# Kernel optimization log

Hardware: AMD Instinct MI355X
Metric: run time of the kernel (lower is better)

Reference implementation:

```python
import jax, jax.numpy as jnp
import numpy as np
from jax import lax

COUNTER_TARGET = 40
CONV_THRESH = 0.01


def compute_ellipticity(images):
    """images: [B,H,W] -> (e1[B], e2[B]) via iterative adaptive-Gaussian moments."""
    B, H, W = images.shape
    y = jnp.arange(H, dtype=jnp.float32) - H / 2.0 + 0.5
    x = jnp.arange(W, dtype=jnp.float32) - W / 2.0 + 0.5
    Y, X = jnp.meshgrid(y, x, indexing='ij')  # [H,W]
    X = X[None]  # [1,H,W]
    Y = Y[None]
    total = jnp.sum(images, axis=(1, 2))
    image_area = jnp.float32(H * W)

    def cond_fn(c):
        i, ax, ay, axy, mux, muy, psxx, psyy, csxx, csyy, back, e1, e2 = c
        first = jnp.equal(i, 0)
        valid = jnp.logical_not(jnp.any(jnp.isnan(csxx))) & jnp.logical_not(jnp.any(jnp.isnan(csyy)))
        converged = (jnp.max(jnp.abs(csxx - psxx)) < CONV_THRESH) & (jnp.max(jnp.abs(csyy - psyy)) < CONV_THRESH)
        converged = converged & jnp.logical_not(first)
        return (i < COUNTER_TARGET) & valid & (first | jnp.logical_not(converged))

    def body_fn(c):
        i, ax, ay, axy, mux, muy, psxx, psyy, csxx, csyy, back, e1, e2 = c
        ax = jnp.clip(ax, 0.5, 20.0)
        ay = jnp.clip(ay, 0.5, 20.0)
        axy = jnp.clip(axy, -10.0, 10.0)
        Xc = X - mux[:, None, None]
        Yc = Y - muy[:, None, None]
        alpha_denom = jnp.maximum(ax * ay, 1e-8)
        alpha_ratio = jnp.clip(axy / alpha_denom, -0.95, 0.95)
        arb_const = jnp.maximum(2.0 * (1.0 - alpha_ratio ** 2), 1e-8)
        sqrt_term = jnp.maximum(1.0 - alpha_ratio ** 2, 1e-8)
        A = 1.0 / (2.0 * jnp.pi * alpha_denom * jnp.sqrt(sqrt_term))
        A = jnp.clip(A, 1e-10, 1e10)
        ax_sq = jnp.maximum(ax ** 2, 1e-8)
        ay_sq = jnp.maximum(ay ** 2, 1e-8)
        e1t = Xc ** 2 / (arb_const * ax_sq)[:, None, None]
        e2t = Yc ** 2 / (arb_const * ay_sq)[:, None, None]
        e3t = 2.0 * axy[:, None, None] * Xc * Yc / (arb_const * ax_sq * ay_sq)[:, None, None]
        exp_term = jnp.clip(e1t + e2t - e3t, 0.0, 30.0)
        k = A[:, None, None] * jnp.exp(-exp_term)
        k = jnp.where(jnp.isnan(k), 0.0, k)
        k = jnp.where(jnp.isinf(k), 0.0, k)
        img1 = images - back[:, None, None]
        ik = img1 * k
        t1 = jnp.sum(X * Y * ik, axis=(1, 2))
        t2 = jnp.sum(ik, axis=(1, 2))
        t3 = jnp.sum(X * ik, axis=(1, 2))
        t4 = jnp.sum(Y * ik, axis=(1, 2))
        t5 = jnp.sum(X * X * ik, axis=(1, 2))
        t6 = jnp.sum(Y * Y * ik, axis=(1, 2))
        t7 = jnp.sum(k * k, axis=(1, 2))
        t2s = jnp.maximum(jnp.abs(t2), 1e-6)
        t7s = jnp.maximum(t7, 1e-6)
        flux_calc = t2 / t7s
        new_back = jnp.clip((total - flux_calc) / image_area, -1.0, 1.0)
        new_mux = jnp.clip(t3 / t2s, -W / 2.0, W / 2.0)
        new_muy = jnp.clip(t4 / t2s, -H / 2.0, H / 2.0)
        sigxx = t5 / t2s - (t3 / t2s) ** 2
        sigyy = t6 / t2s - (t4 / t2s) ** 2
        sigxy = t1 / t2s - t3 * t4 / (t2s * t2s)
        sigxx = jnp.clip(sigxx, 0.25, 100.0)
        sigyy = jnp.clip(sigyy, 0.25, 100.0)
        sigxy = jnp.clip(sigxy, -50.0, 50.0)
        nax = jnp.sqrt(jnp.clip(sigxx * 2.0, 1.0, 400.0))
        nay = jnp.sqrt(jnp.clip(sigyy * 2.0, 1.0, 400.0))
        naxy = jnp.clip(2.0 * sigxy, -20.0, 20.0)
        denom = jnp.maximum(sigxx + sigyy, 1e-6)
        ne1 = jnp.clip((sigxx - sigyy) / denom, -0.95, 0.95)
        ne2 = jnp.clip(2.0 * sigxy / denom, -0.95, 0.95)
        ne1 = jnp.where(jnp.isnan(ne1), 0.0, ne1)
        ne2 = jnp.where(jnp.isnan(ne2), 0.0, ne2)
        nax = jnp.where(jnp.isnan(nax), 2.0, nax)
        nay = jnp.where(jnp.isnan(nay), 2.0, nay)
        naxy = jnp.where(jnp.isnan(naxy), 0.0, naxy)
        return (i + 1, nax, nay, naxy, new_mux, new_muy, csxx, csyy, sigxx, sigyy, new_back, ne1, ne2)

    def step(c, _):
        cont = cond_fn(c)
        nc = body_fn(c)
        c = jax.tree_util.tree_map(lambda a, b: jnp.where(cont, b, a), c, nc)
        return c, None

    init = (jnp.int32(0),
            jnp.full([B], 2.0), jnp.full([B], 2.0), jnp.zeros([B]),
            jnp.zeros([B]), jnp.zeros([B]),
            jnp.full([B], 4.0), jnp.full([B], 4.0),
            jnp.zeros([B]), jnp.zeros([B]),
            jnp.zeros([B]), jnp.zeros([B]), jnp.zeros([B]))
    final, _ = lax.scan(step, init, None, length=COUNTER_TARGET)
    e1, e2 = final[11], final[12]
    e1 = jnp.where(jnp.isnan(e1) | jnp.isinf(e1), 0.0, e1)
    e2 = jnp.where(jnp.isnan(e2) | jnp.isinf(e2), 0.0, e2)
    return e1, e2


def blur_with_kernel(image, kernel):
    """image [B,H,W,1], kernel [B,kH,kW,1] -> per-sample SAME conv (correlation)."""
    def single(img, ker):
        ker = ker / (jnp.sum(ker) + 1e-6)
        ker = ker[..., None]  # [kH,kW,1,1] HWIO
        out = lax.conv_general_dilated(img[None], ker, window_strides=(1, 1),
                                       padding='SAME',
                                       dimension_numbers=('NHWC', 'HWIO', 'NHWC'))
        return out[0]
    return jax.vmap(single)(image, kernel)


def setup_inputs() -> dict:
    key = jax.random.key(0)
    ks = jax.random.split(key, 5)
    B, H, W, kH = 512, 96, 96, 31
    return {
        'y_pred': jax.random.uniform(ks[0], (B, H, W, 1), dtype=jnp.float32),
        'y_true': jax.random.uniform(ks[1], (B, H, W, 1), dtype=jnp.float32),
        'blurred_img': jax.random.uniform(ks[2], (B, H, W, 2), dtype=jnp.float32),
        'kernel_img': jax.random.uniform(ks[3], (B, kH, kH, 1), dtype=jnp.float32),
        'weight_map': jax.random.uniform(ks[4], (B, H, W, 1), dtype=jnp.float32),
        'current_epoch': 3,
    }


def reference(y_pred, y_true, blurred_img, kernel_img, weight_map, current_epoch):
    weighted_mse = jnp.mean(jnp.square(y_pred - y_true) * weight_map)
    sharp_true = jnp.squeeze(y_true, axis=-1)
    sharp_pred = jnp.squeeze(y_pred, axis=-1)
    e1_t, e2_t = compute_ellipticity(sharp_true)
    e1_p, e2_p = compute_ellipticity(sharp_pred)
    ellip_diff = jnp.mean((e1_t - e1_p) ** 2 + (e2_t - e2_p) ** 2)
    ellip_loss = jnp.clip(ellip_diff, 0.0, 1.0)
    ellip_weight = 0.01 + 0.1 * jnp.float32(min(current_epoch, 4))
    original_blurred = blurred_img[:, :, :, 0:1]
    reblurred = blur_with_kernel(y_pred, kernel_img)
    reblur_loss = jnp.mean(jnp.square(reblurred - original_blurred) * weight_map)
    total_loss = 100.0 * weighted_mse + 100.0 * reblur_loss + ellip_weight * ellip_loss
    return total_loss
```

## Files before the change

### kernel.cpp

```cpp
#include <hip/hip_runtime.h>

#define HW 9216
#define NBATCH 512

__device__ __forceinline__ float clampf(float v, float lo, float hi){ return fminf(fmaxf(v, lo), hi); }

__device__ __forceinline__ float waveSum(float v){
#pragma unroll
  for (int o = 32; o; o >>= 1) v += __shfl_xor(v, o, 64);
  return v;
}

__global__ __launch_bounds__(256) void mse_kernel(const float4* __restrict__ yp,
                                                  const float4* __restrict__ yt,
                                                  const float4* __restrict__ wm,
                                                  float* __restrict__ partial){
  __shared__ float red[4];
  const int tid = threadIdx.x;
  int idx = blockIdx.x * 256 + tid;
  float s = 0.f;
#pragma unroll
  for (int u = 0; u < 9; ++u){
    float4 a = yp[idx], b = yt[idx], w = wm[idx];
    float dx = a.x-b.x, dy = a.y-b.y, dz = a.z-b.z, dw = a.w-b.w;
    s += dx*dx*w.x + dy*dy*w.y + dz*dz*w.z + dw*dw*w.w;
    idx += 131072;
  }
  s = waveSum(s);
  if ((tid & 63) == 0) red[tid >> 6] = s;
  __syncthreads();
  if (tid == 0) partial[blockIdx.x] = red[0]+red[1]+red[2]+red[3];
}

__global__ __launch_bounds__(256)
void fused_kernel(const float* __restrict__ y_true,
                  const float* __restrict__ y_pred,
                  const float* __restrict__ kimg,
                  const float* __restrict__ blurred,
                  const float* __restrict__ wmap,
                  float2* __restrict__ ebuf,
                  float* __restrict__ convp){
  __shared__ float smem[7816];
  typedef __fp16 half2_t __attribute__((ext_vector_type(2)));
  const int tid = threadIdx.x;
  const int bid = blockIdx.x;
  const int g   = bid / 5, r5 = bid - g*5;
  const int wave = tid >> 6, lane = tid & 63;

  if (r5 < 2){
    const int id = g*2 + r5;
    float (*wred)[4] = (float(*)[4])smem;
    float* tred = smem + 28;
    const int d = id >> 9;
    const int b = id & 511;
    const int tx = tid & 31, ty = tid >> 5;

    const float* src = (d ? y_pred : y_true) + (size_t)b * HW + ty * 96 + tx;

    unsigned px2[6][3];
    float tot = 0.f;
#pragma unroll
    for (int jj = 0; jj < 6; ++jj){
#pragma unroll
      for (int c = 0; c < 3; ++c){
        float ve = src[jj*1536 + c*32];
        float vo = src[jj*1536 + 768 + c*32];
        tot += ve + vo;
        half2_t pk = __builtin_amdgcn_cvt_pkrtz(ve, vo);
        unsigned u = __builtin_bit_cast(unsigned, pk);
        asm volatile("" : "+v"(u));
        px2[jj][c] = u;
      }
    }
    tot = waveSum(tot);
    if (lane == 0) tred[wave] = tot;
    __syncthreads();
    float total;
    { float4 t = *reinterpret_cast<const float4*>(&tred[0]); total = (t.x+t.y)+(t.z+t.w); }
    __syncthreads();

    const float Ya00 = (float)ty - 47.5f;
    float Xa[3];
#pragma unroll
    for (int c = 0; c < 3; ++c){ Xa[c] = (float)(tx + 32*c) - 47.5f; }

    float zx=4.f, zy=4.f, axy=0.f, mux=0.f, muy=0.f, back=0.f, e1=0.f, e2=0.f;
    const float LOG2E = 1.4426950408889634f;
    const float NQLO  = -43.280851226668906f;

    for (int it = 0; it < 40; ++it){
      float axyc = clampf(axy, -10.f, 10.f);
      float prod = zx*zy;
      float adn  = sqrtf(prod);
      float rca  = __builtin_amdgcn_rcpf(adn);
      float ar   = clampf(axyc*rca, -0.95f, 0.95f);
      float omr  = fmaf(-ar, ar, 1.f);
      float A    = 0.15915494309189535f * rca * __builtin_amdgcn_rsqf(omr);
      float invq = __builtin_amdgcn_rcpf(2.f*omr*prod);
      float a1 = -LOG2E*zy*invq;
      float a2 = -LOG2E*zx*invq;
      float a3 = (2.f*LOG2E)*axyc*invq;
      float cX2[3], cX3[3];
#pragma unroll
      for (int c = 0; c < 3; ++c){
        float Xc = Xa[c] - mux;
        cX2[c] = a1*Xc*Xc;
        cX3[c] = a3*Xc;
      }
      float S0[3] = {0.f,0.f,0.f}, SY[3] = {0.f,0.f,0.f};
      float tYY = 0.f, tkk = 0.f;
#pragma unroll
      for (int jj = 0; jj < 6; ++jj){
        float Yae = Ya00 + 16.f*jj;
        float Yao = Yae + 8.f;
        float Yce = Yae - muy, Yco = Yao - muy;
        float he = a2*Yce*Yce, ho = a2*Yco*Yco;
        float rse = 0.f, rso = 0.f;
#pragma unroll
        for (int c = 0; c < 3; ++c){
          half2_t pk = __builtin_bit_cast(half2_t, px2[jj][c]);
          float pe = (float)pk.x, po = (float)pk.y;
          {
            float nq = fmaf(cX3[c], Yce, he + cX2[c]);
            float e  = __builtin_amdgcn_exp2f(fminf(fmaxf(nq, NQLO), 0.f));
            float ik = (pe - back)*e;
            S0[c] += ik;  SY[c] = fmaf(Yae, ik, SY[c]);  tkk = fmaf(e, e, tkk);  rse += ik;
          }
          {
            float nq = fmaf(cX3[c], Yco, ho + cX2[c]);
            float e  = __builtin_amdgcn_exp2f(fminf(fmaxf(nq, NQLO), 0.f));
            float ik = (po - back)*e;
            S0[c] += ik;  SY[c] = fmaf(Yao, ik, SY[c]);  tkk = fmaf(e, e, tkk);  rso += ik;
          }
        }
        tYY = fmaf(Yae*Yae, rse, fmaf(Yao*Yao, rso, tYY));
      }
      float tik = S0[0]+S0[1]+S0[2];
      float tX  = fmaf(Xa[2],S0[2], fmaf(Xa[1],S0[1], Xa[0]*S0[0]));
      float tXX = fmaf(Xa[2]*Xa[2],S0[2], fmaf(Xa[1]*Xa[1],S0[1], (Xa[0]*Xa[0])*S0[0]));
      float tY  = SY[0]+SY[1]+SY[2];
      float tXY = fmaf(Xa[2],SY[2], fmaf(Xa[1],SY[1], Xa[0]*SY[0]));
      tXY=waveSum(tXY); tik=waveSum(tik); tX=waveSum(tX); tY=waveSum(tY);
      tXX=waveSum(tXX); tYY=waveSum(tYY); tkk=waveSum(tkk);
      if (lane == 0){
        wred[0][wave]=tXY; wred[1][wave]=tik; wred[2][wave]=tX; wred[3][wave]=tY;
        wred[4][wave]=tXX; wred[5][wave]=tYY; wred[6][wave]=tkk;
      }
      __syncthreads();
      float T[7];
#pragma unroll
      for (int k = 0; k < 7; ++k){
        float4 r = *reinterpret_cast<const float4*>(&wred[k][0]);
        T[k] = (r.x+r.y)+(r.z+r.w);
      }
      __syncthreads();
      float T1=T[0]*A, T2=T[1]*A, T3=T[2]*A, T4=T[3]*A, T5=T[4]*A, T6=T[5]*A, T7=T[6]*A*A;
      float t2s = fmaxf(fabsf(T2), 1e-6f);
      float rt2 = __builtin_amdgcn_rcpf(t2s);
      float flux = T2 * __builtin_amdgcn_rcpf(fmaxf(T7, 1e-6f));
      back = clampf((total - flux) * (1.f/9216.f), -1.f, 1.f);
      float r3 = T3*rt2, r4 = T4*rt2;
      mux = clampf(r3, -48.f, 48.f);
      muy = clampf(r4, -48.f, 48.f);
      float sxx = clampf(T5*rt2 - r3*r3, 0.25f, 100.f);
      float syy = clampf(T6*rt2 - r4*r4, 0.25f, 100.f);
      float sxy = clampf(T1*rt2 - T3*T4*rt2*rt2, -50.f, 50.f);
      zx = clampf(sxx*2.f, 1.f, 400.f);
      zy = clampf(syy*2.f, 1.f, 400.f);
      axy = clampf(2.f*sxy, -20.f, 20.f);
      float rden = __builtin_amdgcn_rcpf(sxx+syy);
      e1 = clampf((sxx-syy)*rden, -0.95f, 0.95f);
      e2 = clampf(2.f*sxy*rden, -0.95f, 0.95f);
    }
    if (tid == 0) ebuf[d*512 + b] = make_float2(e1, e2);
  } else {
    const int cid = g*3 + (r5 - 2);
    float* P   = smem;
    float* red = smem + 7812;
    const int b = cid / 3, h = cid - b*3;
    const int R0 = h * 32;

    const float* img = y_pred + (size_t)b * HW;
    for (int u = tid; u < 62*126; u += 256){
      int pr = u / 126, pc = u - pr*126;
      int ir = R0 - 15 + pr, ic = pc - 15;
      float v = 0.f;
      if ((unsigned)ir < 96u && (unsigned)ic < 96u) v = img[ir*96 + ic];
      P[u] = v;
    }
    const float* kb = kimg + (size_t)b * 961;
    float ks = 0.f;
    for (int u = tid; u < 961; u += 256) ks += kb[u];
    ks = waveSum(ks);
    if (lane == 0) red[wave] = ks;
    __syncthreads();
    const float inv = __fdividef(1.f, (red[0]+red[1]+red[2]+red[3]) + 1e-6f);

    const int strip = tid & 15, rg = tid >> 4;
    const int c0 = strip*6;
    const int r0 = R0 + rg*2;
    float acc[2][6];
#pragma unroll
    for (int q = 0; q < 2; ++q){
#pragma unroll
      for (int j = 0; j < 6; ++j) acc[q][j] = 0.f;
    }

#pragma unroll 1
    for (int s = 0; s < 32; ++s){
      const float2* prow = reinterpret_cast<const float2*>(&P[(rg*2 + s)*126 + c0]);
      {
        float w[22];
#pragma unroll
        for (int m = 0; m < 11; ++m){ float2 v = prow[m]; w[2*m]=v.x; w[2*m+1]=v.y; }
#pragma unroll
        for (int q = 0; q < 2; ++q){
          const int dy = s - q;
          if (dy >= 0 && dy <= 30){
            const float* kr = kb + dy*31;
#pragma unroll
            for (int dx = 0; dx < 16; ++dx){
              const float kv = kr[dx];
              acc[q][0] = fmaf(kv, w[dx+0], acc[q][0]);
              acc[q][1] = fmaf(kv, w[dx+1], acc[q][1]);
              acc[q][2] = fmaf(kv, w[dx+2], acc[q][2]);
              acc[q][3] = fmaf(kv, w[dx+3], acc[q][3]);
              acc[q][4] = fmaf(kv, w[dx+4], acc[q][4]);
              acc[q][5] = fmaf(kv, w[dx+5], acc[q][5]);
            }
          }
        }
      }
      {
        float w2[20];
#pragma unroll
        for (int m = 0; m < 10; ++m){ float2 v = prow[8+m]; w2[2*m]=v.x; w2[2*m+1]=v.y; }
#pragma unroll
        for (int q = 0; q < 2; ++q){
          const int dy = s - q;
          if (dy >= 0 && dy <= 30){
            const float* kr = kb + dy*31;
#pragma unroll
            for (int dx = 16; dx < 31; ++dx){
              const float kv = kr[dx];
              acc[q][0] = fmaf(kv, w2[dx-16+0], acc[q][0]);
              acc[q][1] = fmaf(kv, w2[dx-16+1], acc[q][1]);
              acc[q][2] = fmaf(kv, w2[dx-16+2], acc[q][2]);
              acc[q][3] = fmaf(kv, w2[dx-16+3], acc[q][3]);
              acc[q][4] = fmaf(kv, w2[dx-16+4], acc[q][4]);
              acc[q][5] = fmaf(kv, w2[dx-16+5], acc[q][5]);
            }
          }
        }
      }
    }

    float lsum = 0.f;
#pragma unroll
    for (int q = 0; q < 2; ++q){
#pragma unroll
      for (int j = 0; j < 6; ++j){
        const int rr = r0+q, cc = c0+j;
        const size_t pix = (size_t)b*HW + rr*96 + cc;
        float ov = acc[q][j] * inv;
        float dd = ov - blurred[2*pix];
        lsum = fmaf(dd*dd, wmap[pix], lsum);
      }
    }
    lsum = waveSum(lsum);
    __syncthreads();
    if (lane == 0) red[wave] = lsum;
    __syncthreads();
    if (tid == 0) convp[cid] = red[0]+red[1]+red[2]+red[3];
  }
}

__global__ __launch_bounds__(512) void final_kernel(const float* __restrict__ msep,
                                                    const float* __restrict__ convp,
                                                    const float2* __restrict__ ebuf,
                                                    const int* __restrict__ epoch,
                                                    float* __restrict__ out){
  __shared__ float red[3][8];
  const int tid = threadIdx.x, wave = tid >> 6, lane = tid & 63;
  float a = msep[tid];
  float bsum = convp[tid] + convp[512 + tid] + convp[1024 + tid];
  float2 et = ebuf[tid], ep = ebuf[512 + tid];
  float dx = et.x - ep.x, dy = et.y - ep.y;
  float c = dx*dx + dy*dy;
  a = waveSum(a); bsum = waveSum(bsum); c = waveSum(c);
  if (lane == 0){ red[0][wave]=a; red[1][wave]=bsum; red[2][wave]=c; }
  __syncthreads();
  if (tid == 0){
    float sa=0, sb=0, sc=0;
#pragma unroll
    for (int w = 0; w < 8; ++w){ sa+=red[0][w]; sb+=red[1][w]; sc+=red[2][w]; }
    float mse   = sa / 4718592.f;
    float rebl  = sb / 4718592.f;
    float ediff = clampf(sc / 512.f, 0.f, 1.f);
    int e = *epoch; if (e > 4) e = 4;
    float ew = 0.01f + 0.1f * (float)e;
    out[0] = 100.f*mse + 100.f*rebl + ew*ediff;
  }
}

extern "C" void kernel_launch(void* const* d_in, const int* in_sizes, int n_in,
                              void* d_out, int out_size, void* d_ws, size_t ws_size,
                              hipStream_t stream){
  const float* y_pred  = (const float*)d_in[0];
  const float* y_true  = (const float*)d_in[1];
  const float* blurred = (const float*)d_in[2];
  const float* kimg    = (const float*)d_in[3];
  const float* wmap    = (const float*)d_in[4];
  const int*   epoch   = (const int*)d_in[5];
  float* out = (float*)d_out;
  float* ws  = (float*)d_ws;

  float*  msep  = ws;
  float*  convp = ws + 512;
  float2* ebufp = (float2*)(ws + 2048);

  mse_kernel<<<512, 256, 0, stream>>>((const float4*)y_pred, (const float4*)y_true,
                                      (const float4*)wmap, msep);

  fused_kernel<<<2560, 256, 0, stream>>>(y_true, y_pred, kimg, blurred, wmap,
                                         ebufp, convp);

  final_kernel<<<1, 512, 0, stream>>>(msep, convp, ebufp, epoch, out);
}
```

Before: 360.2 us.

## Split fused kernel into ellipticity and conv kernels, fold MSE into conv

The combined block-interleaved kernel is split into two separate launches, one for the ellipticity iterations and one for the reblur convolution. The weighted MSE term moves into the convolution epilogue, reading y_pred from the shared tile and y_true from global memory, which removes the standalone MSE kernel and its separate pass over the inputs. Splitting means each kernel gets its own register and LDS footprint and so its own occupancy, but the two kernels now run one after the other on the stream instead of overlapping within a single grid.

```diff
diff --git a/kernel.cpp b/kernel.cpp
--- a/kernel.cpp
+++ b/kernel.cpp
@@ -11,295 +11,273 @@
   return v;
 }
 
-__global__ __launch_bounds__(256) void mse_kernel(const float4* __restrict__ yp,
-                                                  const float4* __restrict__ yt,
-                                                  const float4* __restrict__ wm,
-                                                  float* __restrict__ partial){
+__global__ __launch_bounds__(256)
+void ellip_kernel(const float* __restrict__ y_true,
+                  const float* __restrict__ y_pred,
+                  float2* __restrict__ ebuf){
+  __shared__ float wred[7][4];
+  __shared__ float tred[4];
+  typedef __fp16 half2_t __attribute__((ext_vector_type(2)));
+  const int tid  = threadIdx.x;
+  const int wave = tid >> 6, lane = tid & 63;
+  const int d = blockIdx.x >> 9;
+  const int b = blockIdx.x & 511;
+  const int tx = tid & 31, ty = tid >> 5;
+
+  const float* src = (d ? y_pred : y_true) + (size_t)b * HW + ty * 96 + tx;
+
+  unsigned px2[6][3];
+  float tot = 0.f;
+#pragma unroll
+  for (int jj = 0; jj < 6; ++jj){
+#pragma unroll
+    for (int c = 0; c < 3; ++c){
+      float ve = src[jj*1536 + c*32];
+      float vo = src[jj*1536 + 768 + c*32];
+      tot += ve + vo;
+      half2_t pk = __builtin_amdgcn_cvt_pkrtz(ve, vo);
+      unsigned u = __builtin_bit_cast(unsigned, pk);
+      asm volatile("" : "+v"(u));
+      px2[jj][c] = u;
+    }
+  }
+  tot = waveSum(tot);
+  if (lane == 0) tred[wave] = tot;
+  __syncthreads();
+  float total;
+  { float4 t = *reinterpret_cast<const float4*>(&tred[0]); total = (t.x+t.y)+(t.z+t.w); }
+  __syncthreads();
+
+  const float Ya00 = (float)ty - 47.5f;
+  float Xa[3];
+#pragma unroll
+  for (int c = 0; c < 3; ++c){ Xa[c] = (float)(tx + 32*c) - 47.5f; }
+
+  float zx=4.f, zy=4.f, axy=0.f, mux=0.f, muy=0.f, back=0.f, e1=0.f, e2=0.f;
+  const float LOG2E = 1.4426950408889634f;
+  const float NQLO  = -43.280851226668906f;
+
+  for (int it = 0; it < 40; ++it){
+    float axyc = clampf(axy, -10.f, 10.f);
+    float prod = zx*zy;
+    float adn  = sqrtf(prod);
+    float rca  = __builtin_amdgcn_rcpf(adn);
+    float ar   = clampf(axyc*rca, -0.95f, 0.95f);
+    float omr  = fmaf(-ar, ar, 1.f);
+    float A    = 0.15915494309189535f * rca * __builtin_amdgcn_rsqf(omr);
+    float invq = __builtin_amdgcn_rcpf(2.f*omr*prod);
+    float a1 = -LOG2E*zy*invq;
+    float a2 = -LOG2E*zx*invq;
+    float a3 = (2.f*LOG2E)*axyc*invq;
+    float cX2[3], cX3[3];
+#pragma unroll
+    for (int c = 0; c < 3; ++c){
+      float Xc = Xa[c] - mux;
+      cX2[c] = a1*Xc*Xc;
+      cX3[c] = a3*Xc;
+    }
+    float S0[3] = {0.f,0.f,0.f}, SY[3] = {0.f,0.f,0.f};
+    float tYY = 0.f, tkk = 0.f;
+#pragma unroll
+    for (int jj = 0; jj < 6; ++jj){
+      float Yae = Ya00 + 16.f*jj;
+      float Yao = Yae + 8.f;
+      float Yce = Yae - muy, Yco = Yao - muy;
+      float he = a2*Yce*Yce, ho = a2*Yco*Yco;
+      float rse = 0.f, rso = 0.f;
+#pragma unroll
+      for (int c = 0; c < 3; ++c){
+        half2_t pk = __builtin_bit_cast(half2_t, px2[jj][c]);
+        float pe = (float)pk.x, po = (float)pk.y;
+        {
+          float nq = fmaf(cX3[c], Yce, he + cX2[c]);
+          float e  = __builtin_amdgcn_exp2f(fminf(fmaxf(nq, NQLO), 0.f));
+          float ik = (pe - back)*e;
+          S0[c] += ik;  SY[c] = fmaf(Yae, ik, SY[c]);  tkk = fmaf(e, e, tkk);  rse += ik;
+        }
+        {
+          float nq = fmaf(cX3[c], Yco, ho + cX2[c]);
+          float e  = __builtin_amdgcn_exp2f(fminf(fmaxf(nq, NQLO), 0.f));
+          float ik = (po - back)*e;
+          S0[c] += ik;  SY[c] = fmaf(Yao, ik, SY[c]);  tkk = fmaf(e, e, tkk);  rso += ik;
+        }
+      }
+      tYY = fmaf(Yae*Yae, rse, fmaf(Yao*Yao, rso, tYY));
+    }
+    float tik = S0[0]+S0[1]+S0[2];
+    float tX  = fmaf(Xa[2],S0[2], fmaf(Xa[1],S0[1], Xa[0]*S0[0]));
+    float tXX = fmaf(Xa[2]*Xa[2],S0[2], fmaf(Xa[1]*Xa[1],S0[1], (Xa[0]*Xa[0])*S0[0]));
+    float tY  = SY[0]+SY[1]+SY[2];
+    float tXY = fmaf(Xa[2],SY[2], fmaf(Xa[1],SY[1], Xa[0]*SY[0]));
+    tXY=waveSum(tXY); tik=waveSum(tik); tX=waveSum(tX); tY=waveSum(tY);
+    tXX=waveSum(tXX); tYY=waveSum(tYY); tkk=waveSum(tkk);
+    if (lane == 0){
+      wred[0][wave]=tXY; wred[1][wave]=tik; wred[2][wave]=tX; wred[3][wave]=tY;
+      wred[4][wave]=tXX; wred[5][wave]=tYY; wred[6][wave]=tkk;
+    }
+    __syncthreads();
+    float T[7];
+#pragma unroll
+    for (int k = 0; k < 7; ++k){
+      float4 r = *reinterpret_cast<const float4*>(&wred[k][0]);
+      T[k] = (r.x+r.y)+(r.z+r.w);
+    }
+    __syncthreads();
+    float T1=T[0]*A, T2=T[1]*A, T3=T[2]*A, T4=T[3]*A, T5=T[4]*A, T6=T[5]*A, T7=T[6]*A*A;
+    float t2s = fmaxf(fabsf(T2), 1e-6f);
+    float rt2 = __builtin_amdgcn_rcpf(t2s);
+    float flux = T2 * __builtin_amdgcn_rcpf(fmaxf(T7, 1e-6f));
+    back = clampf((total - flux) * (1.f/9216.f), -1.f, 1.f);
+    float r3 = T3*rt2, r4 = T4*rt2;
+    mux = clampf(r3, -48.f, 48.f);
+    muy = clampf(r4, -48.f, 48.f);
+    float sxx = clampf(T5*rt2 - r3*r3, 0.25f, 100.f);
+    float syy = clampf(T6*rt2 - r4*r4, 0.25f, 100.f);
+    float sxy = clampf(T1*rt2 - T3*T4*rt2*rt2, -50.f, 50.f);
+    zx = clampf(sxx*2.f, 1.f, 400.f);
+    zy = clampf(syy*2.f, 1.f, 400.f);
+    axy = clampf(2.f*sxy, -20.f, 20.f);
+    float rden = __builtin_amdgcn_rcpf(sxx+syy);
+    e1 = clampf((sxx-syy)*rden, -0.95f, 0.95f);
+    e2 = clampf(2.f*sxy*rden, -0.95f, 0.95f);
+  }
+  if (tid == 0) ebuf[d*512 + b] = make_float2(e1, e2);
+}
+
+__global__ __launch_bounds__(256)
+void conv_mse_kernel(const float* __restrict__ y_pred,
+                     const float* __restrict__ y_true,
+                     const float* __restrict__ kimg,
+                     const float* __restrict__ blurred,
+                     const float* __restrict__ wmap,
+                     float* __restrict__ partial){
+  __shared__ float P[62*126];
   __shared__ float red[4];
   const int tid = threadIdx.x;
-  int idx = blockIdx.x * 256 + tid;
-  float s = 0.f;
-#pragma unroll
-  for (int u = 0; u < 9; ++u){
-    float4 a = yp[idx], b = yt[idx], w = wm[idx];
-    float dx = a.x-b.x, dy = a.y-b.y, dz = a.z-b.z, dw = a.w-b.w;
-    s += dx*dx*w.x + dy*dy*w.y + dz*dz*w.z + dw*dw*w.w;
-    idx += 131072;
-  }
-  s = waveSum(s);
-  if ((tid & 63) == 0) red[tid >> 6] = s;
-  __syncthreads();
-  if (tid == 0) partial[blockIdx.x] = red[0]+red[1]+red[2]+red[3];
-}
-
-__global__ __launch_bounds__(256)
-void fused_kernel(const float* __restrict__ y_true,
-                  const float* __restrict__ y_pred,
-                  const float* __restrict__ kimg,
-                  const float* __restrict__ blurred,
-                  const float* __restrict__ wmap,
-                  float2* __restrict__ ebuf,
-                  float* __restrict__ convp){
-  __shared__ float smem[7816];
-  typedef __fp16 half2_t __attribute__((ext_vector_type(2)));
-  const int tid = threadIdx.x;
-  const int bid = blockIdx.x;
-  const int g   = bid / 5, r5 = bid - g*5;
+  const int cid = blockIdx.x;
+  const int b = cid / 3, h = cid - b*3;
+  const int R0 = h * 32;
   const int wave = tid >> 6, lane = tid & 63;
 
-  if (r5 < 2){
-    const int id = g*2 + r5;
-    float (*wred)[4] = (float(*)[4])smem;
-    float* tred = smem + 28;
-    const int d = id >> 9;
-    const int b = id & 511;
-    const int tx = tid & 31, ty = tid >> 5;
-
-    const float* src = (d ? y_pred : y_true) + (size_t)b * HW + ty * 96 + tx;
-
-    unsigned px2[6][3];
-    float tot = 0.f;
-#pragma unroll
-    for (int jj = 0; jj < 6; ++jj){
-#pragma unroll
-      for (int c = 0; c < 3; ++c){
-        float ve = src[jj*1536 + c*32];
-        float vo = src[jj*1536 + 768 + c*32];
-        tot += ve + vo;
-        half2_t pk = __builtin_amdgcn_cvt_pkrtz(ve, vo);
-        unsigned u = __builtin_bit_cast(unsigned, pk);
-        asm volatile("" : "+v"(u));
-        px2[jj][c] = u;
-      }
-    }
-    tot = waveSum(tot);
-    if (lane == 0) tred[wave] = tot;
-    __syncthreads();
-    float total;
-    { float4 t = *reinterpret_cast<const float4*>(&tred[0]); total = (t.x+t.y)+(t.z+t.w); }
-    __syncthreads();
-
-    const float Ya00 = (float)ty - 47.5f;
-    float Xa[3];
-#pragma unroll
-    for (int c = 0; c < 3; ++c){ Xa[c] = (float)(tx + 32*c) - 47.5f; }
-
-    float zx=4.f, zy=4.f, axy=0.f, mux=0.f, muy=0.f, back=0.f, e1=0.f, e2=0.f;
-    const float LOG2E = 1.4426950408889634f;
-    const float NQLO  = -43.280851226668906f;
-
-    for (int it = 0; it < 40; ++it){
-      float axyc = clampf(axy, -10.f, 10.f);
-      float prod = zx*zy;
-      float adn  = sqrtf(prod);
-      float rca  = __builtin_amdgcn_rcpf(adn);
-      float ar   = clampf(axyc*rca, -0.95f, 0.95f);
-      float omr  = fmaf(-ar, ar, 1.f);
-      float A    = 0.15915494309189535f * rca * __builtin_amdgcn_rsqf(omr);
-      float invq = __builtin_amdgcn_rcpf(2.f*omr*prod);
-      float a1 = -LOG2E*zy*invq;
-      float a2 = -LOG2E*zx*invq;
-      float a3 = (2.f*LOG2E)*axyc*invq;
-      float cX2[3], cX3[3];
-#pragma unroll
-      for (int c = 0; c < 3; ++c){
-        float Xc = Xa[c] - mux;
-        cX2[c] = a1*Xc*Xc;
-        cX3[c] = a3*Xc;
-      }
-      float S0[3] = {0.f,0.f,0.f}, SY[3] = {0.f,0.f,0.f};
-      float tYY = 0.f, tkk = 0.f;
-#pragma unroll
-      for (int jj = 0; jj < 6; ++jj){
-        float Yae = Ya00 + 16.f*jj;
-        float Yao = Yae + 8.f;
-        float Yce = Yae - muy, Yco = Yao - muy;
-        float he = a2*Yce*Yce, ho = a2*Yco*Yco;
-        float rse = 0.f, rso = 0.f;
-#pragma unroll
-        for (int c = 0; c < 3; ++c){
-          half2_t pk = __builtin_bit_cast(half2_t, px2[jj][c]);
-          float pe = (float)pk.x, po = (float)pk.y;
-          {
-            float nq = fmaf(cX3[c], Yce, he + cX2[c]);
-            float e  = __builtin_amdgcn_exp2f(fminf(fmaxf(nq, NQLO), 0.f));
-            float ik = (pe - back)*e;
-            S0[c] += ik;  SY[c] = fmaf(Yae, ik, SY[c]);  tkk = fmaf(e, e, tkk);  rse += ik;
-          }
-          {
-            float nq = fmaf(cX3[c], Yco, ho + cX2[c]);
-            float e  = __builtin_amdgcn_exp2f(fminf(fmaxf(nq, NQLO), 0.f));
-            float ik = (po - back)*e;
-            S0[c] += ik;  SY[c] = fmaf(Yao, ik, SY[c]);  tkk = fmaf(e, e, tkk);  rso += ik;
-          }
-        }
-        tYY = fmaf(Yae*Yae, rse, fmaf(Yao*Yao, rso, tYY));
-      }
-      float tik = S0[0]+S0[1]+S0[2];
-      float tX  = fmaf(Xa[2],S0[2], fmaf(Xa[1],S0[1], Xa[0]*S0[0]));
-      float tXX = fmaf(Xa[2]*Xa[2],S0[2], fmaf(Xa[1]*Xa[1],S0[1], (Xa[0]*Xa[0])*S0[0]));
-      float tY  = SY[0]+SY[1]+SY[2];
-      float tXY = fmaf(Xa[2],SY[2], fmaf(Xa[1],SY[1], Xa[0]*SY[0]));
-      tXY=waveSum(tXY); tik=waveSum(tik); tX=waveSum(tX); tY=waveSum(tY);
-      tXX=waveSum(tXX); tYY=waveSum(tYY); tkk=waveSum(tkk);
-      if (lane == 0){
-        wred[0][wave]=tXY; wred[1][wave]=tik; wred[2][wave]=tX; wred[3][wave]=tY;
-        wred[4][wave]=tXX; wred[5][wave]=tYY; wred[6][wave]=tkk;
-      }
-      __syncthreads();
-      float T[7];
-#pragma unroll
-      for (int k = 0; k < 7; ++k){
-        float4 r = *reinterpret_cast<const float4*>(&wred[k][0]);
-        T[k] = (r.x+r.y)+(r.z+r.w);
-      }
-      __syncthreads();
-      float T1=T[0]*A, T2=T[1]*A, T3=T[2]*A, T4=T[3]*A, T5=T[4]*A, T6=T[5]*A, T7=T[6]*A*A;
-      float t2s = fmaxf(fabsf(T2), 1e-6f);
-      float rt2 = __builtin_amdgcn_rcpf(t2s);
-      float flux = T2 * __builtin_amdgcn_rcpf(fmaxf(T7, 1e-6f));
-      back = clampf((total - flux) * (1.f/9216.f), -1.f, 1.f);
-      float r3 = T3*rt2, r4 = T4*rt2;
-      mux = clampf(r3, -48.f, 48.f);
-      muy = clampf(r4, -48.f, 48.f);
-      float sxx = clampf(T5*rt2 - r3*r3, 0.25f, 100.f);
-      float syy = clampf(T6*rt2 - r4*r4, 0.25f, 100.f);
-      float sxy = clampf(T1*rt2 - T3*T4*rt2*rt2, -50.f, 50.f);
-      zx = clampf(sxx*2.f, 1.f, 400.f);
-      zy = clampf(syy*2.f, 1.f, 400.f);
-      axy = clampf(2.f*sxy, -20.f, 20.f);
-      float rden = __builtin_amdgcn_rcpf(sxx+syy);
-      e1 = clampf((sxx-syy)*rden, -0.95f, 0.95f);
-      e2 = clampf(2.f*sxy*rden, -0.95f, 0.95f);
-    }
-    if (tid == 0) ebuf[d*512 + b] = make_float2(e1, e2);
-  } else {
-    const int cid = g*3 + (r5 - 2);
-    float* P   = smem;
-    float* red = smem + 7812;
-    const int b = cid / 3, h = cid - b*3;
-    const int R0 = h * 32;
-
-    const float* img = y_pred + (size_t)b * HW;
-    for (int u = tid; u < 62*126; u += 256){
-      int pr = u / 126, pc = u - pr*126;
-      int ir = R0 - 15 + pr, ic = pc - 15;
-      float v = 0.f;
-      if ((unsigned)ir < 96u && (unsigned)ic < 96u) v = img[ir*96 + ic];
-      P[u] = v;
-    }
-    const float* kb = kimg + (size_t)b * 961;
-    float ks = 0.f;
-    for (int u = tid; u < 961; u += 256) ks += kb[u];
-    ks = waveSum(ks);
-    if (lane == 0) red[wave] = ks;
-    __syncthreads();
-    const float inv = __fdividef(1.f, (red[0]+red[1]+red[2]+red[3]) + 1e-6f);
-
-    const int strip = tid & 15, rg = tid >> 4;
-    const int c0 = strip*6;
-    const int r0 = R0 + rg*2;
-    float acc[2][6];
-#pragma unroll
-    for (int q = 0; q < 2; ++q){
-#pragma unroll
-      for (int j = 0; j < 6; ++j) acc[q][j] = 0.f;
-    }
+  const float* img = y_pred + (size_t)b * HW;
+  for (int u = tid; u < 62*126; u += 256){
+    int pr = u / 126, pc = u - pr*126;
+    int ir = R0 - 15 + pr, ic = pc - 15;
+    float v = 0.f;
+    if ((unsigned)ir < 96u && (unsigned)ic < 96u) v = img[ir*96 + ic];
+    P[u] = v;
+  }
+  const float* kb = kimg + (size_t)b * 961;
+  float ks = 0.f;
+  for (int u = tid; u < 961; u += 256) ks += kb[u];
+  ks = waveSum(ks);
+  if (lane == 0) red[wave] = ks;
+  __syncthreads();
+  const float inv = __fdividef(1.f, (red[0]+red[1]+red[2]+red[3]) + 1e-6f);
+
+  const int strip = tid & 15, rg = tid >> 4;
+  const int c0 = strip*6;
+  const int r0 = R0 + rg*2;
+  float acc[2][6];
+#pragma unroll
+  for (int q = 0; q < 2; ++q){
+#pragma unroll
+    for (int j = 0; j < 6; ++j) acc[q][j] = 0.f;
+  }
 
 #pragma unroll 1
-    for (int s = 0; s < 32; ++s){
-      const float2* prow = reinterpret_cast<const float2*>(&P[(rg*2 + s)*126 + c0]);
-      {
-        float w[22];
-#pragma unroll
-        for (int m = 0; m < 11; ++m){ float2 v = prow[m]; w[2*m]=v.x; w[2*m+1]=v.y; }
-#pragma unroll
-        for (int q = 0; q < 2; ++q){
-          const int dy = s - q;
-          if (dy >= 0 && dy <= 30){
-            const float* kr = kb + dy*31;
-#pragma unroll
-            for (int dx = 0; dx < 16; ++dx){
-              const float kv = kr[dx];
-              acc[q][0] = fmaf(kv, w[dx+0], acc[q][0]);
-              acc[q][1] = fmaf(kv, w[dx+1], acc[q][1]);
-              acc[q][2] = fmaf(kv, w[dx+2], acc[q][2]);
-              acc[q][3] = fmaf(kv, w[dx+3], acc[q][3]);
-              acc[q][4] = fmaf(kv, w[dx+4], acc[q][4]);
-              acc[q][5] = fmaf(kv, w[dx+5], acc[q][5]);
-            }
+  for (int s = 0; s < 32; ++s){
+    const float2* prow = reinterpret_cast<const float2*>(&P[(rg*2 + s)*126 + c0]);
+    {
+      float w[22];
+#pragma unroll
+      for (int m = 0; m < 11; ++m){ float2 v = prow[m]; w[2*m]=v.x; w[2*m+1]=v.y; }
+#pragma unroll
+      for (int q = 0; q < 2; ++q){
+        const int dy = s - q;
+        if (dy >= 0 && dy <= 30){
+          const float* kr = kb + dy*31;
+#pragma unroll
+          for (int dx = 0; dx < 16; ++dx){
+            const float kv = kr[dx];
+            acc[q][0] = fmaf(kv, w[dx+0], acc[q][0]);
+            acc[q][1] = fmaf(kv, w[dx+1], acc[q][1]);
+            acc[q][2] = fmaf(kv, w[dx+2], acc[q][2]);
+            acc[q][3] = fmaf(kv, w[dx+3], acc[q][3]);
+            acc[q][4] = fmaf(kv, w[dx+4], acc[q][4]);
+            acc[q][5] = fmaf(kv, w[dx+5], acc[q][5]);
           }
         }
       }
-      {
-        float w2[20];
-#pragma unroll
-        for (int m = 0; m < 10; ++m){ float2 v = prow[8+m]; w2[2*m]=v.x; w2[2*m+1]=v.y; }
-#pragma unroll
-        for (int q = 0; q < 2; ++q){
-          const int dy = s - q;
-          if (dy >= 0 && dy <= 30){
-            const float* kr = kb + dy*31;
-#pragma unroll
-            for (int dx = 16; dx < 31; ++dx){
-              const float kv = kr[dx];
-              acc[q][0] = fmaf(kv, w2[dx-16+0], acc[q][0]);
-              acc[q][1] = fmaf(kv, w2[dx-16+1], acc[q][1]);
-              acc[q][2] = fmaf(kv, w2[dx-16+2], acc[q][2]);
-              acc[q][3] = fmaf(kv, w2[dx-16+3], acc[q][3]);
-              acc[q][4] = fmaf(kv, w2[dx-16+4], acc[q][4]);
-              acc[q][5] = fmaf(kv, w2[dx-16+5], acc[q][5]);
-            }
+    }
+    {
+      float w2[20];
+#pragma unroll
+      for (int m = 0; m < 10; ++m){ float2 v = prow[8+m]; w2[2*m]=v.x; w2[2*m+1]=v.y; }
+#pragma unroll
+      for (int q = 0; q < 2; ++q){
+        const int dy = s - q;
+        if (dy >= 0 && dy <= 30){
+          const float* kr = kb + dy*31;
+#pragma unroll
+          for (int dx = 16; dx < 31; ++dx){
+            const float kv = kr[dx];
+            acc[q][0] = fmaf(kv, w2[dx-16+0], acc[q][0]);
+            acc[q][1] = fmaf(kv, w2[dx-16+1], acc[q][1]);
+            acc[q][2] = fmaf(kv, w2[dx-16+2], acc[q][2]);
+            acc[q][3] = fmaf(kv, w2[dx-16+3], acc[q][3]);
+            acc[q][4] = fmaf(kv, w2[dx-16+4], acc[q][4]);
+            acc[q][5] = fmaf(kv, w2[dx-16+5], acc[q][5]);
           }
         }
       }
     }
-
-    float lsum = 0.f;
-#pragma unroll
-    for (int q = 0; q < 2; ++q){
-#pragma unroll
-      for (int j = 0; j < 6; ++j){
-        const int rr = r0+q, cc = c0+j;
-        const size_t pix = (size_t)b*HW + rr*96 + cc;
-        float ov = acc[q][j] * inv;
-        float dd = ov - blurred[2*pix];
-        lsum = fmaf(dd*dd, wmap[pix], lsum);
-      }
-    }
-    lsum = waveSum(lsum);
-    __syncthreads();
-    if (lane == 0) red[wave] = lsum;
-    __syncthreads();
-    if (tid == 0) convp[cid] = red[0]+red[1]+red[2]+red[3];
-  }
-}
-
-__global__ __launch_bounds__(512) void final_kernel(const float* __restrict__ msep,
-                                                    const float* __restrict__ convp,
+  }
+
+  float lsum = 0.f;
+#pragma unroll
+  for (int q = 0; q < 2; ++q){
+#pragma unroll
+    for (int j = 0; j < 6; ++j){
+      const int rr = r0+q, cc = c0+j;
+      const size_t pix = (size_t)b*HW + rr*96 + cc;
+      float wv = wmap[pix];
+      float ov = acc[q][j] * inv;
+      float dd = ov - blurred[2*pix];
+      float yv = P[(rg*2 + q + 15)*126 + (cc + 15)];
+      float md = yv - y_true[pix];
+      lsum = fmaf(dd*dd + md*md, wv, lsum);
+    }
+  }
+  lsum = waveSum(lsum);
+  __syncthreads();
+  if (lane == 0) red[wave] = lsum;
+  __syncthreads();
+  if (tid == 0) partial[cid] = red[0]+red[1]+red[2]+red[3];
+}
+
+__global__ __launch_bounds__(512) void final_kernel(const float* __restrict__ convp,
                                                     const float2* __restrict__ ebuf,
                                                     const int* __restrict__ epoch,
                                                     float* __restrict__ out){
-  __shared__ float red[3][8];
+  __shared__ float red[2][8];
   const int tid = threadIdx.x, wave = tid >> 6, lane = tid & 63;
-  float a = msep[tid];
   float bsum = convp[tid] + convp[512 + tid] + convp[1024 + tid];
   float2 et = ebuf[tid], ep = ebuf[512 + tid];
   float dx = et.x - ep.x, dy = et.y - ep.y;
   float c = dx*dx + dy*dy;
-  a = waveSum(a); bsum = waveSum(bsum); c = waveSum(c);
-  if (lane == 0){ red[0][wave]=a; red[1][wave]=bsum; red[2][wave]=c; }
+  bsum = waveSum(bsum); c = waveSum(c);
+  if (lane == 0){ red[0][wave]=bsum; red[1][wave]=c; }
   __syncthreads();
   if (tid == 0){
-    float sa=0, sb=0, sc=0;
-#pragma unroll
-    for (int w = 0; w < 8; ++w){ sa+=red[0][w]; sb+=red[1][w]; sc+=red[2][w]; }
-    float mse   = sa / 4718592.f;
-    float rebl  = sb / 4718592.f;
+    float sb=0, sc=0;
+#pragma unroll
+    for (int w = 0; w < 8; ++w){ sb+=red[0][w]; sc+=red[1][w]; }
+    float both  = sb / 4718592.f;
     float ediff = clampf(sc / 512.f, 0.f, 1.f);
     int e = *epoch; if (e > 4) e = 4;
     float ew = 0.01f + 0.1f * (float)e;
-    out[0] = 100.f*mse + 100.f*rebl + ew*ediff;
+    out[0] = 100.f*both + ew*ediff;
   }
 }
 
@@ -315,15 +293,12 @@
   float* out = (float*)d_out;
   float* ws  = (float*)d_ws;
 
-  float*  msep  = ws;
-  float*  convp = ws + 512;
-  float2* ebufp = (float2*)(ws + 2048);
-
-  mse_kernel<<<512, 256, 0, stream>>>((const float4*)y_pred, (const float4*)y_true,
-                                      (const float4*)wmap, msep);
-
-  fused_kernel<<<2560, 256, 0, stream>>>(y_true, y_pred, kimg, blurred, wmap,
-                                         ebufp, convp);
-
-  final_kernel<<<1, 512, 0, stream>>>(msep, convp, ebufp, epoch, out);
-}
+  float*  convp = ws;
+  float2* ebufp = (float2*)(ws + 1536);
+
+  ellip_kernel<<<1024, 256, 0, stream>>>(y_true, y_pred, ebufp);
+
+  conv_mse_kernel<<<1536, 256, 0, stream>>>(y_pred, y_true, kimg, blurred, wmap, convp);
+
+  final_kernel<<<1, 512, 0, stream>>>(convp, ebufp, epoch, out);
+}
```

After: 311.7 us. -13.5%, faster.
